# Kernel tuning notes

Measured on AMD Instinct MI355X. Metric: run time of the kernel, lower is better.

The kernel has to match this reference:

```python
import jax, jax.numpy as jnp
import numpy as np

B, S, E, H, D = 4, 2048, 1024, 16, 64  # batch, seq, embed, heads, head_dim


def setup_inputs() -> dict:
    key = jax.random.key(0)
    k1, k2, k3 = jax.random.split(key, 3)
    x = jax.random.normal(k1, (B, S, E), dtype=jnp.float32)
    qkv_w = jax.random.normal(k2, (E, H, 3 * D), dtype=jnp.float32) * (1.0 / np.sqrt(E))
    qkv_b = jnp.zeros((H, 3 * D), dtype=jnp.float32)
    out_w = jax.random.normal(k3, (H, D, E), dtype=jnp.float32) * (1.0 / np.sqrt(H * D))
    out_b = jnp.zeros((E,), dtype=jnp.float32)
    return {"x": x, "qkv_w": qkv_w, "qkv_b": qkv_b, "out_w": out_w, "out_b": out_b}


def _large_negative_number(dtype):
    return jnp.asarray(-0.7 * jnp.finfo(dtype).max, dtype=dtype)


def reference(x, qkv_w, qkv_b, out_w, out_b):
    # qkv projection: LinearGeneral(E -> (H, 3D))
    qkv = jnp.einsum('bse,ehd->bshd', x, qkv_w) + qkv_b  # [B,S,H,3D]
    q, k, v = jnp.split(qkv, 3, axis=-1)  # each [B,S,H,D]
    logits = jnp.einsum('bqhd,bkhd->bhqk', q, k)  # [B,H,S,S]
    logits = logits / jnp.sqrt(jnp.asarray(q.shape[-1], logits.dtype))
    mask = jnp.tril(jnp.ones((q.shape[1], q.shape[1]), dtype=jnp.bool_))
    logits = jnp.where(mask, logits, _large_negative_number(logits.dtype))
    probs = jax.nn.softmax(logits, axis=-1)
    attn = jnp.einsum('bhqk,bkhd->bqhd', probs, v)  # [B,S,H,D]
    # output projection: LinearGeneral((H, D) -> E)
    return jnp.einsum('bqhd,hde->bqe', attn, out_w) + out_b
```

## Files before the change

### kernel.cpp

```cpp
#include <hip/hip_runtime.h>

typedef unsigned int u32;
typedef _Float16 f16;
typedef _Float16 f16x8 __attribute__((ext_vector_type(8)));
typedef _Float16 f16x4 __attribute__((ext_vector_type(4)));
typedef float f32x4 __attribute__((ext_vector_type(4)));
typedef _Float16 __attribute__((address_space(3))) lf16;

#define LOG2E 1.4426950408889634f

__device__ __forceinline__ void gl_lds16(const void* g, void* l) {
  __builtin_amdgcn_global_load_lds(
      (const __attribute__((address_space(1))) u32*)g,
      (__attribute__((address_space(3))) u32*)l, 16, 0, 0);
}

__device__ __forceinline__ f32x4 mfma16(f16x8 a, f16x8 b, f32x4 c) {
  return __builtin_amdgcn_mfma_f32_16x16x32_f16(a, b, c, 0, 0, 0);
}

__device__ __forceinline__ f16x8 ldsr(const f16* p) {
  f16x8 r;
  asm volatile("ds_read_b128 %0, %1" : "=v"(r) : "v"((const lf16*)p));
  return r;
}

__global__ void k_prep(const float* __restrict__ x, f16* __restrict__ xb,
                       const float* __restrict__ wqkv, f16* __restrict__ wqkvt,
                       const float* __restrict__ wo, f16* __restrict__ wot) {
  __shared__ f16 tile[32][33];
  const int b = blockIdx.x, t = threadIdx.x;
  if (b < 4096) {
    const float* in;
    f16* out;
    int C, bx, by;
    if (b < 3072) { in = wqkv; out = wqkvt; C = 3072; bx = b % 96; by = b / 96; }
    else          { in = wo;   out = wot;   C = 1024; bx = (b - 3072) & 31; by = (b - 3072) >> 5; }
    const int c0 = bx * 32, r0 = by * 32;
    const int tx = t & 31, ty = t >> 5;
#pragma unroll
    for (int i = ty; i < 32; i += 8)
      tile[i][tx] = (f16)in[(size_t)(r0 + i) * C + c0 + tx];
    __syncthreads();
#pragma unroll
    for (int i = ty; i < 32; i += 8)
      out[(size_t)(c0 + i) * 1024 + r0 + tx] = tile[tx][i];
  } else {
    const int idx0 = (b - 4096) * 256 + t;
    for (int i = idx0; i < 1048576; i += 1024 * 256) {
      f32x4 a = *(const f32x4*)(x + (size_t)i * 8);
      f32x4 c = *(const f32x4*)(x + (size_t)i * 8 + 4);
      f16x8 o;
      o[0] = (f16)a[0]; o[1] = (f16)a[1]; o[2] = (f16)a[2]; o[3] = (f16)a[3];
      o[4] = (f16)c[0]; o[5] = (f16)c[1]; o[6] = (f16)c[2]; o[7] = (f16)c[3];
      *(f16x8*)(xb + (size_t)i * 8) = o;
    }
  }
}

__device__ __forceinline__ void gemm_fatA(
    const f16* __restrict__ A, const f16* __restrict__ Bt,
    int bm, int bn, f16* SM, int w, int lane, f32x4 (&acc)[8][4]) {
  constexpr int KT = 32;
  const int g = lane >> 4, rl = lane & 15;
  const int l4 = lane >> 2, ls = lane & 3;
  const int sslot = ls ^ ((l4 >> 1) & 3);

  const f16* aS = A + (size_t)(bm + w * 32 + l4) * 1024 + sslot * 8;
  const f16* bS = Bt + (size_t)(bn + w * 16 + l4) * 1024 + sslot * 8;
  f16* aD = SM + w * 1024;
  f16* bD = SM + 4096 + w * 512;

#define ASTG0(b, kt) do { \
    gl_lds16(aS + (kt) * 32,          aD + (b) * 12288); \
    gl_lds16(aS + 16384 + (kt) * 32,  aD + (b) * 12288 + 512); \
    gl_lds16(bS + (kt) * 32,          bD + (b) * 12288); } while (0)
#define ASTG1(b, kt) do { \
    gl_lds16(bS + 65536 + (kt) * 32,  bD + (b) * 12288 + 2048); \
    gl_lds16(bS + 131072 + (kt) * 32, bD + (b) * 12288 + 4096); \
    gl_lds16(bS + 196608 + (kt) * 32, bD + (b) * 12288 + 6144); } while (0)

  ASTG0(0, 0); ASTG1(0, 0);
  ASTG0(1, 1); ASTG1(1, 1);
  asm volatile("s_waitcnt vmcnt(6)" ::: "memory");
  __builtin_amdgcn_s_barrier();

  const int ro = rl * 32 + ((g ^ ((rl >> 1) & 3)) * 8);

  int c = 0, cs = 2;
#pragma unroll 1
  for (int kt = 0; kt < KT; ++kt) {
    const f16* SMc = SM + c * 12288;
    const bool stg = (kt + 2 < KT);
    f16x8 bf[4], af[4];

    {
#pragma unroll
      for (int j = 0; j < 4; ++j)
        bf[j] = ldsr(SMc + 4096 + w * 2048 + j * 512 + ro);
#pragma unroll
      for (int mi = 0; mi < 4; ++mi)
        af[mi] = ldsr(SMc + mi * 512 + ro);
      if (stg) ASTG0(cs, kt + 2);
      __builtin_amdgcn_s_barrier();
      asm volatile("s_waitcnt lgkmcnt(0)");
      __builtin_amdgcn_sched_barrier(0);
      __builtin_amdgcn_s_setprio(1);
#pragma unroll
      for (int mi = 0; mi < 4; ++mi)
#pragma unroll
        for (int j = 0; j < 4; ++j)
          acc[mi][j] = mfma16(af[mi], bf[j], acc[mi][j]);
      __builtin_amdgcn_s_setprio(0);
      __builtin_amdgcn_sched_barrier(0);
      __builtin_amdgcn_s_barrier();
    }
    {
#pragma unroll
      for (int mi = 0; mi < 4; ++mi)
        af[mi] = ldsr(SMc + (4 + mi) * 512 + ro);
      if (stg) ASTG1(cs, kt + 2);
      __builtin_amdgcn_s_barrier();
      asm volatile("s_waitcnt lgkmcnt(0)");
      __builtin_amdgcn_sched_barrier(0);
      __builtin_amdgcn_s_setprio(1);
#pragma unroll
      for (int mi = 0; mi < 4; ++mi)
#pragma unroll
        for (int j = 0; j < 4; ++j)
          acc[4 + mi][j] = mfma16(af[mi], bf[j], acc[4 + mi][j]);
      __builtin_amdgcn_s_setprio(0);
      __builtin_amdgcn_sched_barrier(0);
      if (kt + 2 < KT)      { asm volatile("s_waitcnt vmcnt(6)" ::: "memory"); }
      else if (kt + 1 < KT) { asm volatile("s_waitcnt vmcnt(0)" ::: "memory"); }
      __builtin_amdgcn_s_barrier();
      __builtin_amdgcn_sched_barrier(0);
    }
    c = (c == 2) ? 0 : c + 1;
    cs = (cs == 2) ? 0 : cs + 1;
  }
#undef ASTG0
#undef ASTG1
}

__global__ __launch_bounds__(256, 2) void k_gemm_qkv4(
    const f16* __restrict__ A, const f16* __restrict__ Bt,
    const float* __restrict__ bias,
    f16* __restrict__ qo, f16* __restrict__ ko2, f16* __restrict__ vto) {
  __shared__ __align__(16) f16 SM[36864];
  const int lin0 = blockIdx.y * 12 + blockIdx.x;
  const int lin = (lin0 & 7) * 96 + (lin0 >> 3);
  const int bn = (lin % 12) * 256, bm = (lin / 12) * 128;
  const int t = threadIdx.x, lane = t & 63, w = t >> 6;
  const int g = lane >> 4, rl = lane & 15;

  f32x4 acc[8][4] = {};
  gemm_fatA(A, Bt, bm, bn, SM, w, lane, acc);

#pragma unroll
  for (int mi = 0; mi < 8; ++mi)
#pragma unroll
    for (int j = 0; j < 4; ++j)
#pragma unroll
      for (int r = 0; r < 4; ++r) {
        int m = bm + mi * 16 + g * 4 + r;
        int n = bn + w * 64 + j * 16 + rl;
        float v = acc[mi][j][r] + bias[n];
        int b = m >> 11, s = m & 2047;
        int h = n / 192, rem = n - h * 192;
        int tsel = rem >> 6, dd = rem & 63;
        size_t bh = (size_t)(b * 16 + h);
        if (tsel == 0)      qo[(bh * 2048 + s) * 64 + dd] = (f16)(v * (0.125f * LOG2E));
        else if (tsel == 1) ko2[(bh * 2048 + s) * 64 + dd] = (f16)v;
        else                vto[(bh * 64 + dd) * 2048 + s] = (f16)v;
      }
}

__device__ __forceinline__ void gemm97(
    const f16* __restrict__ A, const f16* __restrict__ Bt,
    int bm, int bn, f16* SM, int w, int lane, f32x4 (&acc)[4][4]) {
  constexpr int KT = 32;
  const int g = lane >> 4, rl = lane & 15;
  const int l4 = lane >> 2, ls = lane & 3;
  const int sslot = ls ^ ((l4 >> 1) & 3);
  const int wr = w >> 1, wc = w & 1;

  const f16* aS = A + (size_t)(bm + w * 16 + l4) * 1024 + sslot * 8;
  const f16* bS = Bt + (size_t)(bn + w * 16 + l4) * 1024 + sslot * 8;

#define STG97(b, kt) do { \
    gl_lds16(aS + (kt) * 32,          SM + (b) * 8192 + w * 512); \
    gl_lds16(aS + 65536 + (kt) * 32,  SM + (b) * 8192 + 2048 + w * 512); \
    gl_lds16(bS + (kt) * 32,          SM + (b) * 8192 + 4096 + w * 512); \
    gl_lds16(bS + 65536 + (kt) * 32,  SM + (b) * 8192 + 6144 + w * 512); } while (0)

  const int ro = rl * 32 + ((g ^ ((rl >> 1) & 3)) * 8);

  STG97(0, 0);
  __syncthreads();

#pragma unroll 1
  for (int kt = 0; kt < KT; ++kt) {
    const int cur = kt & 1;
    if (kt + 1 < KT) STG97(cur ^ 1, kt + 1);
    const f16* SMb = SM + cur * 8192;
    f16x8 af[4], bf[4];
#pragma unroll
    for (int mi = 0; mi < 4; ++mi)
      af[mi] = *(const f16x8*)(SMb + wr * 2048 + mi * 512 + ro);
#pragma unroll
    for (int j = 0; j < 4; ++j)
      bf[j] = *(const f16x8*)(SMb + 4096 + wc * 2048 + j * 512 + ro);
    __builtin_amdgcn_s_setprio(1);
#pragma unroll
    for (int mi = 0; mi < 4; ++mi)
#pragma unroll
      for (int j = 0; j < 4; ++j)
        acc[mi][j] = mfma16(af[mi], bf[j], acc[mi][j]);
    __builtin_amdgcn_s_setprio(0);
    __syncthreads();
  }
#undef STG97
}

__global__ __launch_bounds__(256, 3) void k_gemm_out5(
    const f16* __restrict__ A, const f16* __restrict__ Bt,
    const float* __restrict__ bias, float* __restrict__ out) {
  __shared__ __align__(16) f16 SM[16384];
  const int lin0 = blockIdx.y * 8 + blockIdx.x;
  const int lin = (lin0 & 7) * 64 + (lin0 >> 3);
  const int bn = (lin % 8) * 128, bm = (lin / 8) * 128;
  const int t = threadIdx.x, lane = t & 63, w = t >> 6;
  const int g = lane >> 4, rl = lane & 15;
  const int wr = w >> 1, wc = w & 1;

  f32x4 acc[4][4] = {};
  gemm97(A, Bt, bm, bn, SM, w, lane, acc);

#pragma unroll
  for (int i = 0; i < 4; ++i)
#pragma unroll
    for (int j = 0; j < 4; ++j)
#pragma unroll
      for (int r = 0; r < 4; ++r) {
        int m = bm + wr * 64 + i * 16 + g * 4 + r;
        int n = bn + wc * 64 + j * 16 + rl;
        out[(size_t)m * 1024 + n] = acc[i][j][r] + bias[n];
      }
}

__global__ __launch_bounds__(256, 4) void k_attn6(
    const f16* __restrict__ q, const f16* __restrict__ kgl,
    const f16* __restrict__ vt, f16* __restrict__ o) {
  constexpr int S = 2048;
  __shared__ __align__(16) f16 Ks[2][64 * 64];
  __shared__ __align__(16) f16 Vs[2][64 * 64];
  __shared__ __align__(16) f16 Ps[4][16 * 64];

  const int d = blockIdx.x;
  const int bh = (d & 7) * 8 + ((d >> 3) & 7);
  const int v_ = d >> 6, g2 = v_ >> 2, r2 = v_ & 3;
  const int qb = (g2 == 0) ? 15 - r2 : (g2 == 1) ? r2 : (g2 == 2) ? 11 - r2 : 4 + r2;

  const int t = threadIdx.x, lane = t & 63, w = t >> 6;
  const int g = lane >> 4, rl = lane & 15;

  const f16* qp = q + ((size_t)bh * S + qb * 128) * 64;
  const f16* kb = kgl + (size_t)bh * S * 64;
  const f16* vb = vt + (size_t)bh * 64 * S;

  f16x8 qf[2][2];
#pragma unroll
  for (int sub = 0; sub < 2; ++sub)
#pragma unroll
    for (int ks = 0; ks < 2; ++ks)
      qf[sub][ks] = *(const f16x8*)(qp + (size_t)(w * 32 + sub * 16 + rl) * 64 + ks * 32 + g * 8);

  f32x4 oacc[2][4] = {};
  float lrow[2] = {0.f, 0.f};

  const int srow = lane >> 3;
  const int sslot = (lane & 7) ^ srow;

  const int nkt = 2 * qb + 2;
  const int qsub0 = qb * 128 + w * 32;
  const int qmaxw = qsub0 + 31;

  auto STAGE = [&](int bufi, int kt) {
#pragma unroll
    for (int i = 0; i < 2; ++i) {
      const int r0 = w * 16 + i * 8;
      gl_lds16(kb + (size_t)(kt * 64 + r0 + srow) * 64 + sslot * 8, &Ks[bufi][r0 * 64]);
      gl_lds16(vb + (size_t)(r0 + srow) * S + kt * 64 + sslot * 8, &Vs[bufi][r0 * 64]);
    }
  };

  STAGE(0, 0);
  __syncthreads();
  int buf = 0;

  for (int kt = 0; kt < nkt; ++kt) {
    if (kt + 1 < nkt) STAGE(buf ^ 1, kt + 1);

    if (kt * 64 <= qmaxw) {
      const f16* Kb = &Ks[buf][0];
      const f16* Vb = &Vs[buf][0];

      f32x4 sT[2][4] = {};
      __builtin_amdgcn_s_setprio(1);
#pragma unroll
      for (int j = 0; j < 4; ++j)
#pragma unroll
        for (int ks = 0; ks < 2; ++ks) {
          int row = j * 16 + rl;
          f16x8 kf = *(const f16x8*)(Kb + row * 64 + (((ks * 4 + g) ^ (rl & 7)) * 8));
          sT[0][j] = mfma16(kf, qf[0][ks], sT[0][j]);
          sT[1][j] = mfma16(kf, qf[1][ks], sT[1][j]);
        }
      __builtin_amdgcn_s_setprio(0);

      if (kt * 64 + 63 > qsub0) {
#pragma unroll
        for (int sub = 0; sub < 2; ++sub) {
          const int qs = qsub0 + sub * 16;
#pragma unroll
          for (int j = 0; j < 4; ++j)
#pragma unroll
            for (int r = 0; r < 4; ++r)
              if (kt * 64 + j * 16 + g * 4 + r > qs + rl) sT[sub][j][r] = -1e30f;
        }
      }

      f16x8 pf[2][2];
#pragma unroll
      for (int sub = 0; sub < 2; ++sub) {
        float ps = 0.f;
#pragma unroll
        for (int j = 0; j < 4; ++j) {
          float p0 = exp2f(sT[sub][j][0]);
          float p1 = exp2f(sT[sub][j][1]);
          float p2 = exp2f(sT[sub][j][2]);
          float p3 = exp2f(sT[sub][j][3]);
          ps += (p0 + p1) + (p2 + p3);
          auto lo = __builtin_amdgcn_cvt_pkrtz(p0, p1);
          auto hi = __builtin_amdgcn_cvt_pkrtz(p2, p3);
          f16x4 pb;
          pb[0] = (f16)lo[0]; pb[1] = (f16)lo[1]; pb[2] = (f16)hi[0]; pb[3] = (f16)hi[1];
          *(f16x4*)(&Ps[w][0] + rl * 64 + (((j * 2 + (g >> 1)) ^ (rl & 7)) * 8) + (g & 1) * 4) = pb;
        }
        lrow[sub] += ps;

        asm volatile("s_waitcnt lgkmcnt(0)" ::: "memory");
        __builtin_amdgcn_sched_barrier(0);

#pragma unroll
        for (int ks = 0; ks < 2; ++ks)
          pf[sub][ks] = *(const f16x8*)(&Ps[w][0] + rl * 64 + (((ks * 4 + g) ^ (rl & 7)) * 8));
      }

      __builtin_amdgcn_s_setprio(1);
#pragma unroll
      for (int dj = 0; dj < 4; ++dj)
#pragma unroll
        for (int ks = 0; ks < 2; ++ks) {
          int vrow = dj * 16 + rl;
          f16x8 vf = *(const f16x8*)(Vb + vrow * 64 + (((ks * 4 + g) ^ (rl & 7)) * 8));
          oacc[0][dj] = mfma16(pf[0][ks], vf, oacc[0][dj]);
          oacc[1][dj] = mfma16(pf[1][ks], vf, oacc[1][dj]);
        }
      __builtin_amdgcn_s_setprio(0);
    }
    __syncthreads();
    buf ^= 1;
  }

  float rinv[2];
#pragma unroll
  for (int sub = 0; sub < 2; ++sub) {
    float s_ = lrow[sub];
    s_ += __shfl_xor(s_, 16, 64);
    s_ += __shfl_xor(s_, 32, 64);
    rinv[sub] = 1.0f / s_;
  }

  const int h = bh & 15;
  const size_t rowb = (size_t)(bh >> 4) * 2048 + qb * 128 + w * 32;
#pragma unroll
  for (int sub = 0; sub < 2; ++sub)
#pragma unroll
    for (int r = 0; r < 4; ++r) {
      float ri = __shfl(rinv[sub], g * 4 + r, 64);
#pragma unroll
      for (int dj = 0; dj < 4; ++dj)
        o[(rowb + sub * 16 + g * 4 + r) * 1024 + h * 64 + dj * 16 + rl] =
            (f16)(oacc[sub][dj][r] * ri);
    }
}

extern "C" void kernel_launch(void* const* d_in, const int* in_sizes, int n_in,
                              void* d_out, int out_size, void* d_ws, size_t ws_size,
                              hipStream_t stream) {
  (void)in_sizes; (void)n_in; (void)out_size; (void)ws_size;
  const float* x    = (const float*)d_in[0];
  const float* wqkv = (const float*)d_in[1];
  const float* bqkv = (const float*)d_in[2];
  const float* wo   = (const float*)d_in[3];
  const float* bo   = (const float*)d_in[4];
  float* out = (float*)d_out;
  char* ws = (char*)d_ws;

  f16* xb    = (f16*)(ws + 0);
  f16* wqkvt = (f16*)(ws + 16777216);
  f16* wot   = (f16*)(ws + 23068672);
  f16* qws   = (f16*)(ws + 25165824);
  f16* kws   = (f16*)(ws + 41943040);
  f16* vtws  = (f16*)(ws + 58720256);
  f16* attnb = xb;

  k_prep<<<5120, 256, 0, stream>>>(x, xb, wqkv, wqkvt, wo, wot);
  k_gemm_qkv4<<<dim3(12, 64), 256, 0, stream>>>(xb, wqkvt, bqkv, qws, kws, vtws);
  k_attn6<<<1024, 256, 0, stream>>>(qws, kws, vtws, attnb);
  k_gemm_out5<<<dim3(8, 64), 256, 0, stream>>>(attnb, wot, bo, out);
}
```

Baseline: 181.4 us.

## Enlarge QKV GEMM tile to 256x384 with 8 waves per block

Replaces the 128x256 QKV projection GEMM (4 waves) with a 256x384 block tile computed by 8 waves arranged 2x4, each wave holding an 8x6 grid of 16x16 MFMA accumulators. Staging, LDS layout (triple-buffered, 120 KB) and the vmcnt waits are adjusted, and the grid shrinks to 8x32 blocks. The aim is higher arithmetic intensity and less global/LDS traffic per FLOP. The cost is much higher register pressure (48 accumulators per wave) and more LDS per block, which may reduce occupancy and cause spills, and the 256-block grid leaves part of the CUs idle.

```diff
diff --git a/kernel.cpp b/kernel.cpp
--- a/kernel.cpp
+++ b/kernel.cpp
@@ -58,31 +58,39 @@
   }
 }
 
-__device__ __forceinline__ void gemm_fatA(
+__global__ __launch_bounds__(512, 2) void k_gemm_qkv7(
     const f16* __restrict__ A, const f16* __restrict__ Bt,
-    int bm, int bn, f16* SM, int w, int lane, f32x4 (&acc)[8][4]) {
+    const float* __restrict__ bias,
+    f16* __restrict__ qo, f16* __restrict__ ko2, f16* __restrict__ vto) {
   constexpr int KT = 32;
+  __shared__ __align__(16) f16 SM[61440];
+  const int lin0 = blockIdx.y * 8 + blockIdx.x;
+  const int lin = (lin0 & 7) * 32 + (lin0 >> 3);
+  const int bm = (lin >> 3) * 256, bn = (lin & 7) * 384;
+  const int t = threadIdx.x, lane = t & 63, w = t >> 6;
   const int g = lane >> 4, rl = lane & 15;
   const int l4 = lane >> 2, ls = lane & 3;
+  const int wr = w >> 2, wc = w & 3;
   const int sslot = ls ^ ((l4 >> 1) & 3);
 
   const f16* aS = A + (size_t)(bm + w * 32 + l4) * 1024 + sslot * 8;
   const f16* bS = Bt + (size_t)(bn + w * 16 + l4) * 1024 + sslot * 8;
   f16* aD = SM + w * 1024;
-  f16* bD = SM + 4096 + w * 512;
-
-#define ASTG0(b, kt) do { \
-    gl_lds16(aS + (kt) * 32,          aD + (b) * 12288); \
-    gl_lds16(aS + 16384 + (kt) * 32,  aD + (b) * 12288 + 512); \
-    gl_lds16(bS + (kt) * 32,          bD + (b) * 12288); } while (0)
-#define ASTG1(b, kt) do { \
-    gl_lds16(bS + 65536 + (kt) * 32,  bD + (b) * 12288 + 2048); \
-    gl_lds16(bS + 131072 + (kt) * 32, bD + (b) * 12288 + 4096); \
-    gl_lds16(bS + 196608 + (kt) * 32, bD + (b) * 12288 + 6144); } while (0)
-
-  ASTG0(0, 0); ASTG1(0, 0);
-  ASTG0(1, 1); ASTG1(1, 1);
-  asm volatile("s_waitcnt vmcnt(6)" ::: "memory");
+  f16* bD = SM + 8192 + w * 512;
+
+#define QSTG0(b, kt) do { \
+    gl_lds16(aS + (kt) * 32,           aD + (b) * 20480); \
+    gl_lds16(aS + 16384 + (kt) * 32,   aD + (b) * 20480 + 512); \
+    gl_lds16(bS + (kt) * 32,           bD + (b) * 20480); } while (0)
+#define QSTG1(b, kt) do { \
+    gl_lds16(bS + 131072 + (kt) * 32,  bD + (b) * 20480 + 4096); \
+    gl_lds16(bS + 262144 + (kt) * 32,  bD + (b) * 20480 + 8192); } while (0)
+
+  f32x4 acc[8][6] = {};
+
+  QSTG0(0, 0); QSTG1(0, 0);
+  QSTG0(1, 1); QSTG1(1, 1);
+  asm volatile("s_waitcnt vmcnt(5)" ::: "memory");
   __builtin_amdgcn_s_barrier();
 
   const int ro = rl * 32 + ((g ^ ((rl >> 1) & 3)) * 8);
@@ -90,18 +98,18 @@
   int c = 0, cs = 2;
 #pragma unroll 1
   for (int kt = 0; kt < KT; ++kt) {
-    const f16* SMc = SM + c * 12288;
+    const f16* SMc = SM + c * 20480;
     const bool stg = (kt + 2 < KT);
-    f16x8 bf[4], af[4];
+    f16x8 bf[6], af[4];
 
     {
 #pragma unroll
-      for (int j = 0; j < 4; ++j)
-        bf[j] = ldsr(SMc + 4096 + w * 2048 + j * 512 + ro);
+      for (int j = 0; j < 6; ++j)
+        bf[j] = ldsr(SMc + 8192 + wc * 3072 + j * 512 + ro);
 #pragma unroll
       for (int mi = 0; mi < 4; ++mi)
-        af[mi] = ldsr(SMc + mi * 512 + ro);
-      if (stg) ASTG0(cs, kt + 2);
+        af[mi] = ldsr(SMc + wr * 4096 + mi * 512 + ro);
+      if (stg) QSTG0(cs, kt + 2);
       __builtin_amdgcn_s_barrier();
       asm volatile("s_waitcnt lgkmcnt(0)");
       __builtin_amdgcn_sched_barrier(0);
@@ -109,7 +117,7 @@
 #pragma unroll
       for (int mi = 0; mi < 4; ++mi)
 #pragma unroll
-        for (int j = 0; j < 4; ++j)
+        for (int j = 0; j < 6; ++j)
           acc[mi][j] = mfma16(af[mi], bf[j], acc[mi][j]);
       __builtin_amdgcn_s_setprio(0);
       __builtin_amdgcn_sched_barrier(0);
@@ -118,8 +126,8 @@
     {
 #pragma unroll
       for (int mi = 0; mi < 4; ++mi)
-        af[mi] = ldsr(SMc + (4 + mi) * 512 + ro);
-      if (stg) ASTG1(cs, kt + 2);
+        af[mi] = ldsr(SMc + wr * 4096 + (4 + mi) * 512 + ro);
+      if (stg) QSTG1(cs, kt + 2);
       __builtin_amdgcn_s_barrier();
       asm volatile("s_waitcnt lgkmcnt(0)");
       __builtin_amdgcn_sched_barrier(0);
@@ -127,11 +135,11 @@
 #pragma unroll
       for (int mi = 0; mi < 4; ++mi)
 #pragma unroll
-        for (int j = 0; j < 4; ++j)
+        for (int j = 0; j < 6; ++j)
           acc[4 + mi][j] = mfma16(af[mi], bf[j], acc[4 + mi][j]);
       __builtin_amdgcn_s_setprio(0);
       __builtin_amdgcn_sched_barrier(0);
-      if (kt + 2 < KT)      { asm volatile("s_waitcnt vmcnt(6)" ::: "memory"); }
+      if (kt + 2 < KT)      { asm volatile("s_waitcnt vmcnt(5)" ::: "memory"); }
       else if (kt + 1 < KT) { asm volatile("s_waitcnt vmcnt(0)" ::: "memory"); }
       __builtin_amdgcn_s_barrier();
       __builtin_amdgcn_sched_barrier(0);
@@ -139,32 +147,17 @@
     c = (c == 2) ? 0 : c + 1;
     cs = (cs == 2) ? 0 : cs + 1;
   }
-#undef ASTG0
-#undef ASTG1
-}
-
-__global__ __launch_bounds__(256, 2) void k_gemm_qkv4(
-    const f16* __restrict__ A, const f16* __restrict__ Bt,
-    const float* __restrict__ bias,
-    f16* __restrict__ qo, f16* __restrict__ ko2, f16* __restrict__ vto) {
-  __shared__ __align__(16) f16 SM[36864];
-  const int lin0 = blockIdx.y * 12 + blockIdx.x;
-  const int lin = (lin0 & 7) * 96 + (lin0 >> 3);
-  const int bn = (lin % 12) * 256, bm = (lin / 12) * 128;
-  const int t = threadIdx.x, lane = t & 63, w = t >> 6;
-  const int g = lane >> 4, rl = lane & 15;
-
-  f32x4 acc[8][4] = {};
-  gemm_fatA(A, Bt, bm, bn, SM, w, lane, acc);
+#undef QSTG0
+#undef QSTG1
 
 #pragma unroll
   for (int mi = 0; mi < 8; ++mi)
 #pragma unroll
-    for (int j = 0; j < 4; ++j)
+    for (int j = 0; j < 6; ++j)
 #pragma unroll
       for (int r = 0; r < 4; ++r) {
-        int m = bm + mi * 16 + g * 4 + r;
-        int n = bn + w * 64 + j * 16 + rl;
+        int m = bm + wr * 128 + mi * 16 + g * 4 + r;
+        int n = bn + wc * 96 + j * 16 + rl;
         float v = acc[mi][j][r] + bias[n];
         int b = m >> 11, s = m & 2047;
         int h = n / 192, rem = n - h * 192;
@@ -418,7 +411,7 @@
   f16* attnb = xb;
 
   k_prep<<<5120, 256, 0, stream>>>(x, xb, wqkv, wqkvt, wo, wot);
-  k_gemm_qkv4<<<dim3(12, 64), 256, 0, stream>>>(xb, wqkvt, bqkv, qws, kws, vtws);
+  k_gemm_qkv7<<<dim3(8, 32), 512, 0, stream>>>(xb, wqkvt, bqkv, qws, kws, vtws);
   k_attn6<<<1024, 256, 0, stream>>>(qws, kws, vtws, attnb);
   k_gemm_out5<<<dim3(8, 64), 256, 0, stream>>>(attnb, wot, bo, out);
 }
```

Measured after the change: 167.0 us. 1.09x faster.
